# Kernel tuning notes

Measured on AMD Instinct MI355X. Metric: run time of the kernel, lower is better.

## Reference

```python
import jax, jax.numpy as jnp
import numpy as np

B, S, D, H = 2, 2048, 1024, 16
DH = D // H
MASKED_BIAS = -10000.0


def setup_inputs() -> dict:
    key = jax.random.key(0)
    k1, k2, k3 = jax.random.split(key, 3)
    x = jax.random.normal(k1, (B, S, D), dtype=jnp.float32)
    w_attn = jax.random.normal(k2, (D, 3 * D), dtype=jnp.float32) * 0.02
    b_attn = jnp.zeros((3 * D,), dtype=jnp.float32)
    w_proj = jax.random.normal(k3, (D, D), dtype=jnp.float32) * 0.02
    b_proj = jnp.zeros((D,), dtype=jnp.float32)
    return {"x": x, "w_attn": w_attn, "b_attn": b_attn, "w_proj": w_proj, "b_proj": b_proj}


def reference(x, w_attn, b_attn, w_proj, b_proj):
    # c_attn (Conv1D): [B,S,D] @ [D,3D] + b -> [B,S,3D]
    qkv = x @ w_attn + b_attn
    q, k, v = jnp.split(qkv, 3, axis=-1)

    def split_heads(t):  # [B,S,D] -> [B,H,S,DH]
        return t.reshape(B, S, H, DH).transpose(0, 2, 1, 3)

    q, k, v = split_heads(q), split_heads(k), split_heads(v)

    # scores: [B,H,S,S], scaled by sqrt(head_dim) (value.size(-1))
    scores = jnp.einsum('bhqd,bhkd->bhqk', q, k) / jnp.float32(np.sqrt(DH))

    # causal mask via torch.where against masked_bias (-10000.0), not -inf
    causal = jnp.tril(jnp.ones((S, S), dtype=bool))
    scores = jnp.where(causal, scores, jnp.float32(MASKED_BIAS))

    attn = jax.nn.softmax(scores, axis=-1)  # attn_pdrop = 0 -> dropout is identity
    ctx = jnp.einsum('bhqk,bhkd->bhqd', attn, v)  # [B,H,S,DH]

    # merge heads -> [B,S,D], then c_proj (resid_pdrop = 0)
    ctx = ctx.transpose(0, 2, 1, 3).reshape(B, S, D)
    out = ctx @ w_proj + b_proj
    return out
```

## Files before the change

### kernel.cpp

```cpp
#include <hip/hip_runtime.h>
#include <hip/hip_bf16.h>


#define BB 2
#define SS 2048
#define DD 1024
#define HH 16
#define DHH 64
#define MTOK (BB * SS)
#define N3D (3 * DD)

typedef __attribute__((ext_vector_type(8))) short bf16x8;
typedef __attribute__((ext_vector_type(4))) float f32x4;
typedef __attribute__((ext_vector_type(4))) short short4v;

__device__ __forceinline__ short f2bf(float f) {
  unsigned int x = __float_as_uint(f);
  unsigned int r = (x + 0x7fffu + ((x >> 16) & 1u)) >> 16;
  return (short)r;
}

__device__ __forceinline__ unsigned int cvtpk_bf16(float lo, float hi) {
  unsigned int r;
  asm("v_cvt_pk_bf16_f32 %0, %1, %2" : "=v"(r) : "v"(lo), "v"(hi));
  return r;
}

__global__ void cast_bf16_k(const float* __restrict__ in, short* __restrict__ out, int n4) {
  int i = blockIdx.x * blockDim.x + threadIdx.x;
  if (i < n4) {
    float4 v = reinterpret_cast<const float4*>(in)[i];
    short4v o;
    o[0] = f2bf(v.x); o[1] = f2bf(v.y); o[2] = f2bf(v.z); o[3] = f2bf(v.w);
    reinterpret_cast<short4v*>(out)[i] = o;
  }
}

__global__ void transpose_cast_k(const float* __restrict__ W, short* __restrict__ Wt, int K, int N) {
  __shared__ float t[32][33];
  int n0 = blockIdx.x * 32, k0 = blockIdx.y * 32;
  int tx = threadIdx.x, ty = threadIdx.y;
#pragma unroll
  for (int i = 0; i < 4; ++i)
    t[ty + 8 * i][tx] = W[(size_t)(k0 + ty + 8 * i) * N + n0 + tx];
  __syncthreads();
#pragma unroll
  for (int i = 0; i < 4; ++i)
    Wt[(size_t)(n0 + ty + 8 * i) * K + k0 + tx] = f2bf(t[tx][ty + 8 * i]);
}

__global__ void extract_vt_k(const short* __restrict__ qkv, short* __restrict__ vt) {
  __shared__ short t[32][33];
  int s0 = blockIdx.x * 32, d0 = blockIdx.y * 32;
  int bh = blockIdx.z;
  int b = bh >> 4, h = bh & 15;
  int tx = threadIdx.x, ty = threadIdx.y;
#pragma unroll
  for (int i = 0; i < 4; ++i)
    t[ty + 8 * i][tx] =
        qkv[(size_t)(b * SS + s0 + ty + 8 * i) * N3D + 2 * DD + h * DHH + d0 + tx];
  __syncthreads();
#pragma unroll
  for (int i = 0; i < 4; ++i)
    vt[(size_t)(bh * DHH + d0 + ty + 8 * i) * SS + s0 + tx] = t[tx][ty + 8 * i];
}

template <int OUTF32>
__global__ __launch_bounds__(256) void gemm128_k(const short* __restrict__ A,
                                                 const short* __restrict__ Bt,
                                                 const float* __restrict__ bias,
                                                 void* __restrict__ Cout,
                                                 int M, int N, int K) {
  __shared__ short As[128 * 64];
  __shared__ short Bs[128 * 64];
  int tid = threadIdx.x;
  int m0 = blockIdx.y * 128, n0 = blockIdx.x * 128;
  int w = tid >> 6, lane = tid & 63;
  int wr = w >> 1, wc = w & 1;
  int ln16 = lane & 15, l16 = lane >> 4;

  f32x4 acc[4][4] = {};

  int lrow0 = w * 32 + (lane >> 3);
  int blk_p = lane & 7;

  for (int k0 = 0; k0 < K; k0 += 64) {
#pragma unroll
    for (int i = 0; i < 4; ++i) {
      int row_p = lrow0 + i * 8;
      int colE = ((blk_p ^ (row_p & 7)) << 3);
      __builtin_amdgcn_global_load_lds(
          (const __attribute__((address_space(1))) unsigned int*)&A[(size_t)(m0 + row_p) * K + k0 + colE],
          (__attribute__((address_space(3))) unsigned int*)&As[(w * 4 + i) * 512],
          16, 0, 0);
      __builtin_amdgcn_global_load_lds(
          (const __attribute__((address_space(1))) unsigned int*)&Bt[(size_t)(n0 + row_p) * K + k0 + colE],
          (__attribute__((address_space(3))) unsigned int*)&Bs[(w * 4 + i) * 512],
          16, 0, 0);
    }
    __syncthreads();
#pragma unroll
    for (int kk = 0; kk < 2; ++kk) {
      bf16x8 a[4], bfr[4];
#pragma unroll
      for (int mi = 0; mi < 4; ++mi) {
        int row = wr * 64 + mi * 16 + ln16;
        int blk = (kk * 4 + l16) ^ (row & 7);
        a[mi] = *reinterpret_cast<const bf16x8*>(&As[row * 64 + blk * 8]);
      }
#pragma unroll
      for (int ni = 0; ni < 4; ++ni) {
        int row = wc * 64 + ni * 16 + ln16;
        int blk = (kk * 4 + l16) ^ (row & 7);
        bfr[ni] = *reinterpret_cast<const bf16x8*>(&Bs[row * 64 + blk * 8]);
      }
#pragma unroll
      for (int mi = 0; mi < 4; ++mi)
#pragma unroll
        for (int ni = 0; ni < 4; ++ni)
          acc[mi][ni] = __builtin_amdgcn_mfma_f32_16x16x32_bf16(a[mi], bfr[ni], acc[mi][ni], 0, 0, 0);
    }
    __syncthreads();
  }

#pragma unroll
  for (int mi = 0; mi < 4; ++mi)
#pragma unroll
    for (int ni = 0; ni < 4; ++ni)
#pragma unroll
      for (int ri = 0; ri < 4; ++ri) {
        int row = m0 + wr * 64 + mi * 16 + l16 * 4 + ri;
        int col = n0 + wc * 64 + ni * 16 + ln16;
        float v = acc[mi][ni][ri] + bias[col];
        if (OUTF32)
          reinterpret_cast<float*>(Cout)[(size_t)row * N + col] = v;
        else
          reinterpret_cast<short*>(Cout)[(size_t)row * N + col] = f2bf(v);
      }
}

__global__ __launch_bounds__(512) void flash_attn_k(const short* __restrict__ qkv,
                                                    const short* __restrict__ vt,
                                                    short* __restrict__ ctx) {
  __shared__ short Ks[2][64][72], Vs[2][64][72];
  __shared__ short Ps[8][16][72];
  __shared__ float m1s[4][16], l1s[4][16];

  int tid = threadIdx.x;
  int pj = blockIdx.x;
  int bh = blockIdx.y;
  int b = bh >> 4, h = bh & 15;
  int wg = tid >> 6, lane = tid & 63;
  int g = wg >> 2, w = wg & 3;
  int ln16 = lane & 15, l16 = lane >> 4;
  int t8 = tid & 255;
  int tb = tid >> 8;
  int r0 = t8 >> 3, cc0 = (t8 & 7) << 3;

  const short* kbase = qkv + (size_t)(b * SS) * N3D + DD + h * DHH;
  const short* vbase = vt + (size_t)(bh * DHH) * SS;

#pragma unroll 1
  for (int ti = 0; ti < 2; ++ti) {
    int qt = ti ? pj : 31 - pj;
    int q0 = qt * 64;

    bf16x8 qf[2];
    {
      const short* qrow = qkv + (size_t)(b * SS + q0 + w * 16 + ln16) * N3D + h * DHH;
      qf[0] = *reinterpret_cast<const bf16x8*>(qrow + l16 * 8);
      qf[1] = *reinterpret_cast<const bf16x8*>(qrow + 32 + l16 * 8);
    }
    float m_ = -1e30f, l_ = 0.f;
    f32x4 cacc[4] = {};

    int ns = (qt + 2) >> 1;
    uint4 kr0, kr1, vr0, vr1;
    {
      int kt_s = tb <= qt ? tb : qt;
      kr0 = *reinterpret_cast<const uint4*>(kbase + (size_t)(kt_s * 64 + r0) * N3D + cc0);
      kr1 = *reinterpret_cast<const uint4*>(kbase + (size_t)(kt_s * 64 + r0 + 32) * N3D + cc0);
      vr0 = *reinterpret_cast<const uint4*>(vbase + (size_t)r0 * SS + kt_s * 64 + cc0);
      vr1 = *reinterpret_cast<const uint4*>(vbase + (size_t)(r0 + 32) * SS + kt_s * 64 + cc0);
    }

#pragma unroll 1
    for (int s = 0; s < ns; ++s) {
      *reinterpret_cast<uint4*>(&Ks[tb][r0][cc0]) = kr0;
      *reinterpret_cast<uint4*>(&Ks[tb][r0 + 32][cc0]) = kr1;
      *reinterpret_cast<uint4*>(&Vs[tb][r0][cc0]) = vr0;
      *reinterpret_cast<uint4*>(&Vs[tb][r0 + 32][cc0]) = vr1;
      __syncthreads();

      {
        int kt_n = 2 * (s + 1) + tb;
        if (kt_n > qt) kt_n = qt;
        kr0 = *reinterpret_cast<const uint4*>(kbase + (size_t)(kt_n * 64 + r0) * N3D + cc0);
        kr1 = *reinterpret_cast<const uint4*>(kbase + (size_t)(kt_n * 64 + r0 + 32) * N3D + cc0);
        vr0 = *reinterpret_cast<const uint4*>(vbase + (size_t)r0 * SS + kt_n * 64 + cc0);
        vr1 = *reinterpret_cast<const uint4*>(vbase + (size_t)(r0 + 32) * SS + kt_n * 64 + cc0);
      }

      int kt_c = 2 * s + g;
      if (kt_c <= qt) {
        f32x4 sacc[4] = {};
#pragma unroll
        for (int kk = 0; kk < 2; ++kk)
#pragma unroll
          for (int ni = 0; ni < 4; ++ni) {
            bf16x8 kf = *reinterpret_cast<const bf16x8*>(&Ks[g][ni * 16 + ln16][kk * 32 + l16 * 8]);
            sacc[ni] = __builtin_amdgcn_mfma_f32_16x16x32_bf16(kf, qf[kk], sacc[ni], 0, 0, 0);
          }

        float p[4][4];
        float mx = -1e30f;
        if (kt_c == qt) {
          int qg = q0 + w * 16 + ln16;
#pragma unroll
          for (int ni = 0; ni < 4; ++ni)
#pragma unroll
            for (int ri = 0; ri < 4; ++ri) {
              int kg = kt_c * 64 + ni * 16 + l16 * 4 + ri;
              float v = sacc[ni][ri] * 0.125f;
              if (kg > qg) v = -1e30f;
              p[ni][ri] = v;
              mx = fmaxf(mx, v);
            }
        } else {
#pragma unroll
          for (int ni = 0; ni < 4; ++ni)
#pragma unroll
            for (int ri = 0; ri < 4; ++ri) {
              float v = sacc[ni][ri] * 0.125f;
              p[ni][ri] = v;
              mx = fmaxf(mx, v);
            }
        }
        mx = fmaxf(mx, __shfl_xor(mx, 16));
        mx = fmaxf(mx, __shfl_xor(mx, 32));
        float mn = fmaxf(m_, mx);
        float sc = __expf(m_ - mn);
        float sum = 0.f;
#pragma unroll
        for (int ni = 0; ni < 4; ++ni)
#pragma unroll
          for (int ri = 0; ri < 4; ++ri) {
            float e = __expf(p[ni][ri] - mn);
            p[ni][ri] = e;
            sum += e;
          }
        sum += __shfl_xor(sum, 16);
        sum += __shfl_xor(sum, 32);
        m_ = mn;
        l_ = l_ * sc + sum;

#pragma unroll
        for (int ni = 0; ni < 4; ++ni) {
          uint2 u;
          u.x = cvtpk_bf16(p[ni][0], p[ni][1]);
          u.y = cvtpk_bf16(p[ni][2], p[ni][3]);
          *reinterpret_cast<uint2*>(&Ps[wg][ln16][ni * 16 + l16 * 4]) = u;
        }
        float scr[4];
#pragma unroll
        for (int ri = 0; ri < 4; ++ri) scr[ri] = __shfl(sc, l16 * 4 + ri);
#pragma unroll
        for (int di = 0; di < 4; ++di)
#pragma unroll
          for (int ri = 0; ri < 4; ++ri) cacc[di][ri] *= scr[ri];

        asm volatile("s_waitcnt lgkmcnt(0)" ::: "memory");

#pragma unroll
        for (int kk = 0; kk < 2; ++kk) {
          bf16x8 pa = *reinterpret_cast<const bf16x8*>(&Ps[wg][ln16][kk * 32 + l16 * 8]);
#pragma unroll
          for (int di = 0; di < 4; ++di) {
            bf16x8 vb = *reinterpret_cast<const bf16x8*>(&Vs[g][di * 16 + ln16][kk * 32 + l16 * 8]);
            cacc[di] = __builtin_amdgcn_mfma_f32_16x16x32_bf16(pa, vb, cacc[di], 0, 0, 0);
          }
        }
      }
      __syncthreads();
    }

    float* dump = reinterpret_cast<float*>(&Ps[0][0][0]);
    if (g == 1) {
#pragma unroll
      for (int di = 0; di < 4; ++di)
#pragma unroll
        for (int ri = 0; ri < 4; ++ri)
          dump[w * 1024 + (l16 * 4 + ri) * 64 + di * 16 + ln16] = cacc[di][ri];
      if (l16 == 0) { m1s[w][ln16] = m_; l1s[w][ln16] = l_; }
    }
    __syncthreads();
    if (g == 0) {
      float m1 = m1s[w][ln16], l1 = l1s[w][ln16];
      float mM = fmaxf(m_, m1);
      float e0 = __expf(m_ - mM), e1 = __expf(m1 - mM);
      float inv = 1.f / (l_ * e0 + l1 * e1);
      float e0r[4], e1r[4], ivr[4];
#pragma unroll
      for (int ri = 0; ri < 4; ++ri) {
        int src = l16 * 4 + ri;
        e0r[ri] = __shfl(e0, src);
        e1r[ri] = __shfl(e1, src);
        ivr[ri] = __shfl(inv, src);
      }
#pragma unroll
      for (int di = 0; di < 4; ++di)
#pragma unroll
        for (int ri = 0; ri < 4; ++ri) {
          float a1 = dump[w * 1024 + (l16 * 4 + ri) * 64 + di * 16 + ln16];
          float o = (cacc[di][ri] * e0r[ri] + a1 * e1r[ri]) * ivr[ri];
          int row = q0 + w * 16 + l16 * 4 + ri;
          int col = h * DHH + di * 16 + ln16;
          ctx[(size_t)(b * SS + row) * DD + col] = f2bf(o);
        }
    }
    __syncthreads();
  }
}

extern "C" void kernel_launch(void* const* d_in, const int* in_sizes, int n_in,
                              void* d_out, int out_size, void* d_ws, size_t ws_size,
                              hipStream_t stream) {
  const float* x      = (const float*)d_in[0];
  const float* w_attn = (const float*)d_in[1];
  const float* b_attn = (const float*)d_in[2];
  const float* w_proj = (const float*)d_in[3];
  const float* b_proj = (const float*)d_in[4];
  float* out = (float*)d_out;

  char* ws = (char*)d_ws;
  short* xb     = (short*)(ws);
  short* wattnT = (short*)(ws + 8388608);
  short* wprojT = (short*)(ws + 14680064);
  short* qkv    = (short*)(ws + 16777216);
  short* vt     = (short*)(ws + 41943040);
  short* ctx    = (short*)(ws + 50331648);

  {
    int n4 = (MTOK * DD) / 4;
    cast_bf16_k<<<(n4 + 255) / 256, 256, 0, stream>>>(x, xb, n4);
  }
  transpose_cast_k<<<dim3(N3D / 32, DD / 32), dim3(32, 8), 0, stream>>>(w_attn, wattnT, DD, N3D);
  transpose_cast_k<<<dim3(DD / 32, DD / 32), dim3(32, 8), 0, stream>>>(w_proj, wprojT, DD, DD);
  gemm128_k<0><<<dim3(N3D / 128, MTOK / 128), 256, 0, stream>>>(xb, wattnT, b_attn, qkv, MTOK, N3D, DD);
  extract_vt_k<<<dim3(SS / 32, DHH / 32, BB * HH), dim3(32, 8), 0, stream>>>(qkv, vt);
  flash_attn_k<<<dim3(16, BB * HH), 512, 0, stream>>>(qkv, vt, ctx);
  gemm128_k<1><<<dim3(DD / 128, MTOK / 128), 256, 0, stream>>>(ctx, wprojT, b_proj, out, MTOK, DD, DD);
}
```

Baseline: 130.2 us.

## Split attention KV across four wave groups and add lazy softmax rescaling

The flash attention kernel grows from 512 to 1024 threads. Key tiles shrink from 64 to 32 keys, and four wave groups each process a different key tile per step, then merge their partial outputs and softmax statistics through shared memory. The 1/sqrt(d) scale is folded into the Q projection epilogue, and the running-max rescale of the accumulator is skipped while the new block max stays within 8 of the old one. The aim is more parallelism per block and fewer exp/multiply ops per tile. The cost is a more expensive four-way merge and higher register and LDS pressure per block.

```diff
diff --git a/kernel.cpp b/kernel.cpp
--- a/kernel.cpp
+++ b/kernel.cpp
@@ -132,30 +132,37 @@
         int row = m0 + wr * 64 + mi * 16 + l16 * 4 + ri;
         int col = n0 + wc * 64 + ni * 16 + ln16;
         float v = acc[mi][ni][ri] + bias[col];
-        if (OUTF32)
+        if (OUTF32) {
           reinterpret_cast<float*>(Cout)[(size_t)row * N + col] = v;
-        else
+        } else {
+          if (col < DD) v *= 0.125f;
           reinterpret_cast<short*>(Cout)[(size_t)row * N + col] = f2bf(v);
-      }
-}
-
-__global__ __launch_bounds__(512) void flash_attn_k(const short* __restrict__ qkv,
-                                                    const short* __restrict__ vt,
-                                                    short* __restrict__ ctx) {
-  __shared__ short Ks[2][64][72], Vs[2][64][72];
-  __shared__ short Ps[8][16][72];
-  __shared__ float m1s[4][16], l1s[4][16];
+        }
+      }
+}
+
+#define MASKV -3.0e38f
+__global__ __launch_bounds__(1024, 8) void flash_attn_k(const short* __restrict__ qkv,
+                                                        const short* __restrict__ vt,
+                                                        short* __restrict__ ctx) {
+  __shared__ __align__(16) char smem[61440];
+  short (*Ks)[32][72] = reinterpret_cast<short(*)[32][72]>(smem);
+  short (*Vs)[64][40] = reinterpret_cast<short(*)[64][40]>(smem + 18432);
+  short (*Ps)[16][40] = reinterpret_cast<short(*)[16][40]>(smem + 38912);
+  float (*ml)[4][16][2] = reinterpret_cast<float(*)[4][16][2]>(smem + 59392);
+  float* Od = reinterpret_cast<float*>(smem);
 
   int tid = threadIdx.x;
   int pj = blockIdx.x;
   int bh = blockIdx.y;
   int b = bh >> 4, h = bh & 15;
   int wg = tid >> 6, lane = tid & 63;
-  int g = wg >> 2, w = wg & 3;
+  int g = wg >> 2, wq = wg & 3;
   int ln16 = lane & 15, l16 = lane >> 4;
   int t8 = tid & 255;
   int tb = tid >> 8;
-  int r0 = t8 >> 3, cc0 = (t8 & 7) << 3;
+  int krow = t8 >> 3, kcol = (t8 & 7) << 3;
+  int vrow = t8 >> 2, vcol = (t8 & 3) << 3;
 
   const short* kbase = qkv + (size_t)(b * SS) * N3D + DD + h * DHH;
   const short* vbase = vt + (size_t)(bh * DHH) * SS;
@@ -167,82 +174,91 @@
 
     bf16x8 qf[2];
     {
-      const short* qrow = qkv + (size_t)(b * SS + q0 + w * 16 + ln16) * N3D + h * DHH;
+      const short* qrow = qkv + (size_t)(b * SS + q0 + wq * 16 + ln16) * N3D + h * DHH;
       qf[0] = *reinterpret_cast<const bf16x8*>(qrow + l16 * 8);
       qf[1] = *reinterpret_cast<const bf16x8*>(qrow + 32 + l16 * 8);
     }
     float m_ = -1e30f, l_ = 0.f;
     f32x4 cacc[4] = {};
 
-    int ns = (qt + 2) >> 1;
-    uint4 kr0, kr1, vr0, vr1;
+    int nt32 = 2 * qt + 2;
+    int ns = (nt32 + 3) >> 2;
+
+    uint4 kreg, vreg;
     {
-      int kt_s = tb <= qt ? tb : qt;
-      kr0 = *reinterpret_cast<const uint4*>(kbase + (size_t)(kt_s * 64 + r0) * N3D + cc0);
-      kr1 = *reinterpret_cast<const uint4*>(kbase + (size_t)(kt_s * 64 + r0 + 32) * N3D + cc0);
-      vr0 = *reinterpret_cast<const uint4*>(vbase + (size_t)r0 * SS + kt_s * 64 + cc0);
-      vr1 = *reinterpret_cast<const uint4*>(vbase + (size_t)(r0 + 32) * SS + kt_s * 64 + cc0);
+      int kt0 = tb < nt32 ? tb : nt32 - 1;
+      kreg = *reinterpret_cast<const uint4*>(kbase + (size_t)(kt0 * 32 + krow) * N3D + kcol);
+      vreg = *reinterpret_cast<const uint4*>(vbase + (size_t)vrow * SS + kt0 * 32 + vcol);
     }
 
 #pragma unroll 1
     for (int s = 0; s < ns; ++s) {
-      *reinterpret_cast<uint4*>(&Ks[tb][r0][cc0]) = kr0;
-      *reinterpret_cast<uint4*>(&Ks[tb][r0 + 32][cc0]) = kr1;
-      *reinterpret_cast<uint4*>(&Vs[tb][r0][cc0]) = vr0;
-      *reinterpret_cast<uint4*>(&Vs[tb][r0 + 32][cc0]) = vr1;
+      *reinterpret_cast<uint4*>(&Ks[tb][krow][kcol]) = kreg;
+      *reinterpret_cast<uint4*>(&Vs[tb][vrow][vcol]) = vreg;
       __syncthreads();
 
       {
-        int kt_n = 2 * (s + 1) + tb;
-        if (kt_n > qt) kt_n = qt;
-        kr0 = *reinterpret_cast<const uint4*>(kbase + (size_t)(kt_n * 64 + r0) * N3D + cc0);
-        kr1 = *reinterpret_cast<const uint4*>(kbase + (size_t)(kt_n * 64 + r0 + 32) * N3D + cc0);
-        vr0 = *reinterpret_cast<const uint4*>(vbase + (size_t)r0 * SS + kt_n * 64 + cc0);
-        vr1 = *reinterpret_cast<const uint4*>(vbase + (size_t)(r0 + 32) * SS + kt_n * 64 + cc0);
-      }
-
-      int kt_c = 2 * s + g;
-      if (kt_c <= qt) {
-        f32x4 sacc[4] = {};
+        int kt_n = (s + 1) * 4 + tb;
+        if (kt_n > nt32 - 1) kt_n = nt32 - 1;
+        kreg = *reinterpret_cast<const uint4*>(kbase + (size_t)(kt_n * 32 + krow) * N3D + kcol);
+        vreg = *reinterpret_cast<const uint4*>(vbase + (size_t)vrow * SS + kt_n * 32 + vcol);
+      }
+
+      int kt_c = s * 4 + g;
+      if (kt_c < nt32) {
+        f32x4 sacc[2] = {};
 #pragma unroll
         for (int kk = 0; kk < 2; ++kk)
 #pragma unroll
-          for (int ni = 0; ni < 4; ++ni) {
+          for (int ni = 0; ni < 2; ++ni) {
             bf16x8 kf = *reinterpret_cast<const bf16x8*>(&Ks[g][ni * 16 + ln16][kk * 32 + l16 * 8]);
             sacc[ni] = __builtin_amdgcn_mfma_f32_16x16x32_bf16(kf, qf[kk], sacc[ni], 0, 0, 0);
           }
 
-        float p[4][4];
-        float mx = -1e30f;
-        if (kt_c == qt) {
-          int qg = q0 + w * 16 + ln16;
-#pragma unroll
-          for (int ni = 0; ni < 4; ++ni)
+        float p[2][4];
+        float mx = MASKV;
+        if (kt_c >= 2 * qt) {
+          int qg = q0 + wq * 16 + ln16;
+#pragma unroll
+          for (int ni = 0; ni < 2; ++ni)
 #pragma unroll
             for (int ri = 0; ri < 4; ++ri) {
-              int kg = kt_c * 64 + ni * 16 + l16 * 4 + ri;
-              float v = sacc[ni][ri] * 0.125f;
-              if (kg > qg) v = -1e30f;
+              int kg = kt_c * 32 + ni * 16 + l16 * 4 + ri;
+              float v = (kg > qg) ? MASKV : sacc[ni][ri];
               p[ni][ri] = v;
               mx = fmaxf(mx, v);
             }
         } else {
 #pragma unroll
-          for (int ni = 0; ni < 4; ++ni)
+          for (int ni = 0; ni < 2; ++ni)
 #pragma unroll
             for (int ri = 0; ri < 4; ++ri) {
-              float v = sacc[ni][ri] * 0.125f;
-              p[ni][ri] = v;
-              mx = fmaxf(mx, v);
+              p[ni][ri] = sacc[ni][ri];
+              mx = fmaxf(mx, sacc[ni][ri]);
             }
         }
         mx = fmaxf(mx, __shfl_xor(mx, 16));
         mx = fmaxf(mx, __shfl_xor(mx, 32));
-        float mn = fmaxf(m_, mx);
-        float sc = __expf(m_ - mn);
+
+        int keep = __all(mx <= m_ + 8.0f);
+        float mn = m_;
+        if (!keep) {
+          mn = fmaxf(m_, mx);
+          float sc = __expf(m_ - mn);
+          l_ *= sc;
+          float scr[4];
+#pragma unroll
+          for (int ri = 0; ri < 4; ++ri) scr[ri] = __shfl(sc, l16 * 4 + ri);
+#pragma unroll
+          for (int di = 0; di < 4; ++di)
+#pragma unroll
+            for (int ri = 0; ri < 4; ++ri) cacc[di][ri] *= scr[ri];
+          m_ = mn;
+        }
+
         float sum = 0.f;
 #pragma unroll
-        for (int ni = 0; ni < 4; ++ni)
+        for (int ni = 0; ni < 2; ++ni)
 #pragma unroll
           for (int ri = 0; ri < 4; ++ri) {
             float e = __expf(p[ni][ri] - mn);
@@ -251,69 +267,63 @@
           }
         sum += __shfl_xor(sum, 16);
         sum += __shfl_xor(sum, 32);
-        m_ = mn;
-        l_ = l_ * sc + sum;
-
-#pragma unroll
-        for (int ni = 0; ni < 4; ++ni) {
+        l_ += sum;
+
+#pragma unroll
+        for (int ni = 0; ni < 2; ++ni) {
           uint2 u;
           u.x = cvtpk_bf16(p[ni][0], p[ni][1]);
           u.y = cvtpk_bf16(p[ni][2], p[ni][3]);
           *reinterpret_cast<uint2*>(&Ps[wg][ln16][ni * 16 + l16 * 4]) = u;
         }
-        float scr[4];
-#pragma unroll
-        for (int ri = 0; ri < 4; ++ri) scr[ri] = __shfl(sc, l16 * 4 + ri);
-#pragma unroll
-        for (int di = 0; di < 4; ++di)
-#pragma unroll
-          for (int ri = 0; ri < 4; ++ri) cacc[di][ri] *= scr[ri];
-
         asm volatile("s_waitcnt lgkmcnt(0)" ::: "memory");
 
-#pragma unroll
-        for (int kk = 0; kk < 2; ++kk) {
-          bf16x8 pa = *reinterpret_cast<const bf16x8*>(&Ps[wg][ln16][kk * 32 + l16 * 8]);
-#pragma unroll
-          for (int di = 0; di < 4; ++di) {
-            bf16x8 vb = *reinterpret_cast<const bf16x8*>(&Vs[g][di * 16 + ln16][kk * 32 + l16 * 8]);
-            cacc[di] = __builtin_amdgcn_mfma_f32_16x16x32_bf16(pa, vb, cacc[di], 0, 0, 0);
-          }
+        bf16x8 pa = *reinterpret_cast<const bf16x8*>(&Ps[wg][ln16][l16 * 8]);
+#pragma unroll
+        for (int di = 0; di < 4; ++di) {
+          bf16x8 vb = *reinterpret_cast<const bf16x8*>(&Vs[g][di * 16 + ln16][l16 * 8]);
+          cacc[di] = __builtin_amdgcn_mfma_f32_16x16x32_bf16(pa, vb, cacc[di], 0, 0, 0);
         }
       }
       __syncthreads();
     }
 
-    float* dump = reinterpret_cast<float*>(&Ps[0][0][0]);
-    if (g == 1) {
+    if (l16 == 0) { ml[g][wq][ln16][0] = m_; ml[g][wq][ln16][1] = l_; }
+    if (g > 0) {
 #pragma unroll
       for (int di = 0; di < 4; ++di)
 #pragma unroll
         for (int ri = 0; ri < 4; ++ri)
-          dump[w * 1024 + (l16 * 4 + ri) * 64 + di * 16 + ln16] = cacc[di][ri];
-      if (l16 == 0) { m1s[w][ln16] = m_; l1s[w][ln16] = l_; }
+          Od[((g - 1) * 4 + wq) * 1040 + (l16 * 4 + ri) * 65 + di * 16 + ln16] = cacc[di][ri];
     }
     __syncthreads();
     if (g == 0) {
-      float m1 = m1s[w][ln16], l1 = l1s[w][ln16];
-      float mM = fmaxf(m_, m1);
-      float e0 = __expf(m_ - mM), e1 = __expf(m1 - mM);
-      float inv = 1.f / (l_ * e0 + l1 * e1);
-      float e0r[4], e1r[4], ivr[4];
+      float e[4][4], inv[4];
 #pragma unroll
       for (int ri = 0; ri < 4; ++ri) {
-        int src = l16 * 4 + ri;
-        e0r[ri] = __shfl(e0, src);
-        e1r[ri] = __shfl(e1, src);
-        ivr[ri] = __shfl(inv, src);
+        int r = l16 * 4 + ri;
+        float mM = ml[0][wq][r][0];
+#pragma unroll
+        for (int gg = 1; gg < 4; ++gg) mM = fmaxf(mM, ml[gg][wq][r][0]);
+        float lt = 0.f;
+#pragma unroll
+        for (int gg = 0; gg < 4; ++gg) {
+          float eg = __expf(ml[gg][wq][r][0] - mM);
+          e[ri][gg] = eg;
+          lt += eg * ml[gg][wq][r][1];
+        }
+        inv[ri] = 1.f / lt;
       }
 #pragma unroll
       for (int di = 0; di < 4; ++di)
 #pragma unroll
         for (int ri = 0; ri < 4; ++ri) {
-          float a1 = dump[w * 1024 + (l16 * 4 + ri) * 64 + di * 16 + ln16];
-          float o = (cacc[di][ri] * e0r[ri] + a1 * e1r[ri]) * ivr[ri];
-          int row = q0 + w * 16 + l16 * 4 + ri;
+          float o = cacc[di][ri] * e[ri][0];
+#pragma unroll
+          for (int gg = 1; gg < 4; ++gg)
+            o += Od[(gg - 1) * 4160 + wq * 1040 + (l16 * 4 + ri) * 65 + di * 16 + ln16] * e[ri][gg];
+          o *= inv[ri];
+          int row = q0 + wq * 16 + l16 * 4 + ri;
           int col = h * DHH + di * 16 + ln16;
           ctx[(size_t)(b * SS + row) * DD + col] = f2bf(o);
         }
@@ -348,6 +358,6 @@
   transpose_cast_k<<<dim3(DD / 32, DD / 32), dim3(32, 8), 0, stream>>>(w_proj, wprojT, DD, DD);
   gemm128_k<0><<<dim3(N3D / 128, MTOK / 128), 256, 0, stream>>>(xb, wattnT, b_attn, qkv, MTOK, N3D, DD);
   extract_vt_k<<<dim3(SS / 32, DHH / 32, BB * HH), dim3(32, 8), 0, stream>>>(qkv, vt);
-  flash_attn_k<<<dim3(16, BB * HH), 512, 0, stream>>>(qkv, vt, ctx);
+  flash_attn_k<<<dim3(16, BB * HH), 1024, 0, stream>>>(qkv, vt, ctx);
   gemm128_k<1><<<dim3(DD / 128, MTOK / 128), 256, 0, stream>>>(ctx, wprojT, b_proj, out, MTOK, DD, DD);
 }
```

Result: slower. 145.6 us (+11.8%).

## Fold softmax scale into QKV GEMM, add lazy rescale and swizzled P tile

Applied to the files above, without the earlier changes.

The QKV GEMM epilogue now pre-multiplies Q columns by 1/sqrt(dh), which removes the per-score multiply in attention. The online softmax skips the running-max update and accumulator rescale when the new max stays within a threshold of the current one, adopting the FA4-style lazy rescale. The P staging buffer uses an XOR swizzle to avoid LDS bank conflicts, and the cross-group partial output dump gets a padded stride and shares a single aliased shared-memory arena. The trade-off is that the lazy rescale lets exponentials grow up to e^8 before renormalisation, and Q rounding now happens after scaling.

```diff
diff --git a/kernel.cpp b/kernel.cpp
--- a/kernel.cpp
+++ b/kernel.cpp
@@ -132,30 +132,37 @@
         int row = m0 + wr * 64 + mi * 16 + l16 * 4 + ri;
         int col = n0 + wc * 64 + ni * 16 + ln16;
         float v = acc[mi][ni][ri] + bias[col];
-        if (OUTF32)
+        if (OUTF32) {
           reinterpret_cast<float*>(Cout)[(size_t)row * N + col] = v;
-        else
+        } else {
+          if (col < DD) v *= 0.125f;
           reinterpret_cast<short*>(Cout)[(size_t)row * N + col] = f2bf(v);
-      }
-}
-
+        }
+      }
+}
+
+#define MASKV -3.0e38f
 __global__ __launch_bounds__(512) void flash_attn_k(const short* __restrict__ qkv,
                                                     const short* __restrict__ vt,
                                                     short* __restrict__ ctx) {
-  __shared__ short Ks[2][64][72], Vs[2][64][72];
-  __shared__ short Ps[8][16][72];
-  __shared__ float m1s[4][16], l1s[4][16];
+  __shared__ __align__(16) char smem[53248];
+  short (*Ks)[64][72] = reinterpret_cast<short(*)[64][72]>(smem);
+  short (*Vs)[64][72] = reinterpret_cast<short(*)[64][72]>(smem + 18432);
+  short* Psr = reinterpret_cast<short*>(smem + 36864);
+  float* Od = reinterpret_cast<float*>(smem);
+  float* mls = reinterpret_cast<float*>(smem + 17408);
 
   int tid = threadIdx.x;
   int pj = blockIdx.x;
   int bh = blockIdx.y;
   int b = bh >> 4, h = bh & 15;
   int wg = tid >> 6, lane = tid & 63;
-  int g = wg >> 2, w = wg & 3;
+  int g = wg >> 2, wq = wg & 3;
   int ln16 = lane & 15, l16 = lane >> 4;
   int t8 = tid & 255;
   int tb = tid >> 8;
   int r0 = t8 >> 3, cc0 = (t8 & 7) << 3;
+  int psq = (wg << 10) + (ln16 << 6);
 
   const short* kbase = qkv + (size_t)(b * SS) * N3D + DD + h * DHH;
   const short* vbase = vt + (size_t)(bh * DHH) * SS;
@@ -167,7 +174,7 @@
 
     bf16x8 qf[2];
     {
-      const short* qrow = qkv + (size_t)(b * SS + q0 + w * 16 + ln16) * N3D + h * DHH;
+      const short* qrow = qkv + (size_t)(b * SS + q0 + wq * 16 + ln16) * N3D + h * DHH;
       qf[0] = *reinterpret_cast<const bf16x8*>(qrow + l16 * 8);
       qf[1] = *reinterpret_cast<const bf16x8*>(qrow + 32 + l16 * 8);
     }
@@ -213,16 +220,15 @@
           }
 
         float p[4][4];
-        float mx = -1e30f;
+        float mx = MASKV;
         if (kt_c == qt) {
-          int qg = q0 + w * 16 + ln16;
+          int qg = q0 + wq * 16 + ln16;
 #pragma unroll
           for (int ni = 0; ni < 4; ++ni)
 #pragma unroll
             for (int ri = 0; ri < 4; ++ri) {
               int kg = kt_c * 64 + ni * 16 + l16 * 4 + ri;
-              float v = sacc[ni][ri] * 0.125f;
-              if (kg > qg) v = -1e30f;
+              float v = (kg > qg) ? MASKV : sacc[ni][ri];
               p[ni][ri] = v;
               mx = fmaxf(mx, v);
             }
@@ -231,15 +237,29 @@
           for (int ni = 0; ni < 4; ++ni)
 #pragma unroll
             for (int ri = 0; ri < 4; ++ri) {
-              float v = sacc[ni][ri] * 0.125f;
-              p[ni][ri] = v;
-              mx = fmaxf(mx, v);
+              p[ni][ri] = sacc[ni][ri];
+              mx = fmaxf(mx, sacc[ni][ri]);
             }
         }
         mx = fmaxf(mx, __shfl_xor(mx, 16));
         mx = fmaxf(mx, __shfl_xor(mx, 32));
-        float mn = fmaxf(m_, mx);
-        float sc = __expf(m_ - mn);
+
+        int keep = __all(mx <= m_ + 8.0f);
+        float mn = m_;
+        if (!keep) {
+          mn = fmaxf(m_, mx);
+          float sc = __expf(m_ - mn);
+          l_ *= sc;
+          float scr[4];
+#pragma unroll
+          for (int ri = 0; ri < 4; ++ri) scr[ri] = __shfl(sc, l16 * 4 + ri);
+#pragma unroll
+          for (int di = 0; di < 4; ++di)
+#pragma unroll
+            for (int ri = 0; ri < 4; ++ri) cacc[di][ri] *= scr[ri];
+          m_ = mn;
+        }
+
         float sum = 0.f;
 #pragma unroll
         for (int ni = 0; ni < 4; ++ni)
@@ -251,29 +271,22 @@
           }
         sum += __shfl_xor(sum, 16);
         sum += __shfl_xor(sum, 32);
-        m_ = mn;
-        l_ = l_ * sc + sum;
+        l_ += sum;
 
 #pragma unroll
         for (int ni = 0; ni < 4; ++ni) {
           uint2 u;
           u.x = cvtpk_bf16(p[ni][0], p[ni][1]);
           u.y = cvtpk_bf16(p[ni][2], p[ni][3]);
-          *reinterpret_cast<uint2*>(&Ps[wg][ln16][ni * 16 + l16 * 4]) = u;
-        }
-        float scr[4];
-#pragma unroll
-        for (int ri = 0; ri < 4; ++ri) scr[ri] = __shfl(sc, l16 * 4 + ri);
-#pragma unroll
-        for (int di = 0; di < 4; ++di)
-#pragma unroll
-          for (int ri = 0; ri < 4; ++ri) cacc[di][ri] *= scr[ri];
-
+          int idx = psq + ((((ni << 1) + (l16 >> 1)) ^ (ln16 & 7)) << 3) + ((l16 & 1) << 2);
+          *reinterpret_cast<uint2*>(&Psr[idx]) = u;
+        }
         asm volatile("s_waitcnt lgkmcnt(0)" ::: "memory");
 
 #pragma unroll
         for (int kk = 0; kk < 2; ++kk) {
-          bf16x8 pa = *reinterpret_cast<const bf16x8*>(&Ps[wg][ln16][kk * 32 + l16 * 8]);
+          bf16x8 pa = *reinterpret_cast<const bf16x8*>(
+              &Psr[psq + ((((kk << 2) + l16) ^ (ln16 & 7)) << 3)]);
 #pragma unroll
           for (int di = 0; di < 4; ++di) {
             bf16x8 vb = *reinterpret_cast<const bf16x8*>(&Vs[g][di * 16 + ln16][kk * 32 + l16 * 8]);
@@ -284,18 +297,17 @@
       __syncthreads();
     }
 
-    float* dump = reinterpret_cast<float*>(&Ps[0][0][0]);
     if (g == 1) {
+      if (l16 == 0) { mls[wq * 16 + ln16] = m_; mls[64 + wq * 16 + ln16] = l_; }
 #pragma unroll
       for (int di = 0; di < 4; ++di)
 #pragma unroll
         for (int ri = 0; ri < 4; ++ri)
-          dump[w * 1024 + (l16 * 4 + ri) * 64 + di * 16 + ln16] = cacc[di][ri];
-      if (l16 == 0) { m1s[w][ln16] = m_; l1s[w][ln16] = l_; }
+          Od[wq * 1040 + (l16 * 4 + ri) * 65 + di * 16 + ln16] = cacc[di][ri];
     }
     __syncthreads();
     if (g == 0) {
-      float m1 = m1s[w][ln16], l1 = l1s[w][ln16];
+      float m1 = mls[wq * 16 + ln16], l1 = mls[64 + wq * 16 + ln16];
       float mM = fmaxf(m_, m1);
       float e0 = __expf(m_ - mM), e1 = __expf(m1 - mM);
       float inv = 1.f / (l_ * e0 + l1 * e1);
@@ -311,9 +323,9 @@
       for (int di = 0; di < 4; ++di)
 #pragma unroll
         for (int ri = 0; ri < 4; ++ri) {
-          float a1 = dump[w * 1024 + (l16 * 4 + ri) * 64 + di * 16 + ln16];
+          float a1 = Od[wq * 1040 + (l16 * 4 + ri) * 65 + di * 16 + ln16];
           float o = (cacc[di][ri] * e0r[ri] + a1 * e1r[ri]) * ivr[ri];
-          int row = q0 + w * 16 + l16 * 4 + ri;
+          int row = q0 + wq * 16 + l16 * 4 + ri;
           int col = h * DHH + di * 16 + ln16;
           ctx[(size_t)(b * SS + row) * DD + col] = f2bf(o);
         }
```

After: 127.3 us. 1.02x faster.
